# Kernel tuning notes

Hardware: AMD Instinct MI355X
Metric: run time of the kernel (lower is better)

Reference implementation:

```python
import jax, jax.numpy as jnp
import numpy as np

B, T, I, H, O = 128, 512, 128, 2048, 10

def setup_inputs() -> dict:
    key = jax.random.key(0)
    k = jax.random.split(key, 6)
    # xavier-uniform-like scales
    def xav(key, shape):
        fan_in, fan_out = shape[0], shape[1]
        lim = np.sqrt(6.0 / (fan_in + fan_out)).astype(np.float32)
        return jax.random.uniform(key, shape, jnp.float32, -lim, lim)
    return {
        "x": jax.random.normal(k[0], (B, T, I), jnp.float32),
        "W_hx": xav(k[1], (I, H)),
        "W_hh": xav(k[2], (H, H)),
        "b_h": jnp.zeros((H,), jnp.float32),
        "W_ph": xav(k[3], (H, O)),
        "b_o": jnp.zeros((O,), jnp.float32),
    }

def reference(x, W_hx, W_hh, b_h, W_ph, b_o):
    # x: [B, T, I] -> scan over time, recurrent tanh cell
    xt_seq = jnp.swapaxes(x, 0, 1)  # [T, B, I]
    h0 = jnp.zeros((x.shape[0], W_hh.shape[0]), x.dtype)

    def step(h, xt):
        h_new = jnp.tanh(xt @ W_hx + h @ W_hh + b_h)
        return h_new, None

    h_T, _ = jax.lax.scan(step, h0, xt_seq)
    logits = h_T @ W_ph + b_o  # [B, O]
    return jax.nn.softmax(logits, axis=-1)
```

## Files before the change

kernel.cpp:

```cpp
#include <hip/hip_runtime.h>
#include <stdint.h>


#define B_   128
#define T_   512
#define I_   128
#define H_   2048
#define O_   10
#define KK   2176
#define NWG  256
#define NTHR 512

typedef __attribute__((ext_vector_type(8))) _Float16 f16x8;
typedef __attribute__((ext_vector_type(4))) float    f32x4;
typedef __attribute__((ext_vector_type(4))) int      i32x4;

__device__ __forceinline__ float f16_to_f(unsigned short u) {
    return (float)__builtin_bit_cast(_Float16, u);
}
__device__ __forceinline__ unsigned short f_to_f16(float f) {
    return __builtin_bit_cast(unsigned short, (_Float16)f);
}

__device__ __forceinline__ void st64cc(unsigned short* p, uint64_t v) {
    asm volatile("global_store_dwordx2 %0, %1, off sc0 sc1"
                 :: "v"((uint64_t)(uintptr_t)p), "v"(v) : "memory");
}
__device__ __forceinline__ void stflag(unsigned int* p, uint32_t v) {
    asm volatile("global_store_dword %0, %1, off sc0 sc1"
                 :: "v"((uint64_t)(uintptr_t)p), "v"(v) : "memory");
}
__device__ __forceinline__ uint32_t ldflag(const unsigned int* p) {
    uint32_t v;
    asm volatile("global_load_dword %0, %1, off sc0 sc1"
                 : "=v"(v) : "v"((uint64_t)(uintptr_t)p) : "memory");
    asm volatile("s_waitcnt vmcnt(0)" ::: "memory");
    __builtin_amdgcn_sched_barrier(0);
    return v;
}

#define MFMA16(a, b, c) __builtin_amdgcn_mfma_f32_16x16x32_f16((a), (b), (c), 0, 0, 0)

__global__ void prep_init(unsigned int* flags) {
    for (int i = threadIdx.x; i < 8192; i += blockDim.x) flags[i] = 0u;
}

__global__ void prep_weights(const float* __restrict__ Whh, const float* __restrict__ Whx,
                             unsigned short* __restrict__ Wt) {
    __shared__ float tile[32][33];
    const int kt = blockIdx.x;
    const int nt = blockIdx.y;
    const int tx = threadIdx.x & 31;
    const int ty = threadIdx.x >> 5;
#pragma unroll
    for (int r = ty; r < 32; r += 8) {
        const int k = kt * 32 + r;
        const int n = nt * 32 + tx;
        tile[r][tx] = (k < H_) ? Whh[(size_t)k * H_ + n] : Whx[(size_t)(k - H_) * H_ + n];
    }
    __syncthreads();
#pragma unroll
    for (int r = ty; r < 32; r += 8) {
        const int n = nt * 32 + r;
        const int k = kt * 32 + tx;
        Wt[(size_t)n * KK + k] = f_to_f16(tile[tx][r]);
    }
}

__global__ __launch_bounds__(NTHR, 2) void rnn_scan(
    const float* __restrict__ x,
    const unsigned short* __restrict__ Wt,
    const float* __restrict__ b_h,
    const float* __restrict__ W_ph,
    const float* __restrict__ b_o,
    unsigned short* __restrict__ h0,
    unsigned short* __restrict__ h1,
    float* __restrict__ out,
    unsigned int* __restrict__ flags)
{
    const int tid  = threadIdx.x;
    const int wg   = blockIdx.x;
    const int w    = tid >> 6;
    const int lane = tid & 63;
    const int l15  = lane & 15;
    const int l4   = lane >> 4;
    const int rb   = wg >> 5;
    const int cb   = wg & 31;
    const int r0   = rb * 16;
    const int c0   = cb * 64;
    const int arow = r0 + l15;

    unsigned int* gslots = flags + 16 + (size_t)(rb * 32) * 16;
    unsigned int* myslot = gslots + (size_t)cb * 16;
    unsigned int* prodslot = gslots + (size_t)((w * 4 + (lane & 3)) * 16);

    __shared__ f32x4 red[8][4][64];
    __shared__ unsigned short hT[16][68];
    __shared__ float epi[128];
    __shared__ float lgt[16];

    i32x4 wh[4][8];
    i32x4 wx[4];
#pragma unroll
    for (int n = 0; n < 4; ++n) {
        const size_t colbase = (size_t)(c0 + n * 16 + l15) * KK;
#pragma unroll
        for (int j = 0; j < 8; ++j)
            wh[n][j] = *(const i32x4*)(Wt + colbase + (size_t)(w * 256 + j * 32 + l4 * 8));
        if (w >= 4)
            wx[n] = *(const i32x4*)(Wt + colbase + (size_t)(2048 + (w - 4) * 32 + l4 * 8));
    }

    const int rn   = tid >> 6;
    const int rL   = tid & 63;
    const int lcol = rn * 16 + (rL & 15);
    const int lr0  = (rL >> 4) * 4;
    const float rbias = b_h[c0 + lcol];
    const int slr = tid >> 4;
    const int scg = tid & 15;

    for (int t = 0; t < T_; ++t) {
        const unsigned short* rh  = (t & 1) ? h0 : h1;
        unsigned short*       whp = (t & 1) ? h1 : h0;

        f32x4 acc[4];
#pragma unroll
        for (int n = 0; n < 4; ++n) acc[n] = f32x4{0.f, 0.f, 0.f, 0.f};

        if (w >= 4) {
            const float* xp = x + ((size_t)arow * T_ + t) * I_ + (size_t)((w - 4) * 32 + l4 * 8);
            const f32x4 xa = *(const f32x4*)xp;
            const f32x4 xb = *(const f32x4*)(xp + 4);
            f16x8 xv;
#pragma unroll
            for (int jj = 0; jj < 8; ++jj)
                xv[jj] = (_Float16)((jj < 4) ? xa[jj] : xb[jj - 4]);
#pragma unroll
            for (int n = 0; n < 4; ++n)
                acc[n] = MFMA16(xv, __builtin_bit_cast(f16x8, wx[n]), acc[n]);
        }

        if (t > 0) {
            for (;;) {
                uint32_t v = 0xFFFFFFFFu;
                if ((lane & ~3) == 0) v = ldflag(prodslot);
                if (__all((int)(v >= (unsigned)t))) break;
            }

            const uint64_t base64 = (uint64_t)(uintptr_t)(rh + (size_t)arow * H_ + (size_t)(w * 256 + l4 * 8));
            i32x4 hb[8];
#define ISSJ(jj, IMM) \
    asm volatile("global_load_dwordx4 %0, %1, off offset:" IMM " sc1" \
                 : "=v"(hb[jj]) : "v"(base64) : "memory")
#define WAITV(NSTR) do { \
    asm volatile("s_waitcnt vmcnt(" NSTR ")" ::: "memory"); \
    __builtin_amdgcn_sched_barrier(0); } while (0)
#define CONS(jj) do { \
    const f16x8 AH = __builtin_bit_cast(f16x8, hb[jj]); \
    acc[0] = MFMA16(AH, __builtin_bit_cast(f16x8, wh[0][jj]), acc[0]); \
    acc[1] = MFMA16(AH, __builtin_bit_cast(f16x8, wh[1][jj]), acc[1]); \
    acc[2] = MFMA16(AH, __builtin_bit_cast(f16x8, wh[2][jj]), acc[2]); \
    acc[3] = MFMA16(AH, __builtin_bit_cast(f16x8, wh[3][jj]), acc[3]); \
    } while (0)
            ISSJ(0, "0");   ISSJ(1, "64");  ISSJ(2, "128"); ISSJ(3, "192");
            ISSJ(4, "256"); ISSJ(5, "320"); ISSJ(6, "384"); ISSJ(7, "448");
            WAITV("7"); CONS(0);
            WAITV("6"); CONS(1);
            WAITV("5"); CONS(2);
            WAITV("4"); CONS(3);
            WAITV("3"); CONS(4);
            WAITV("2"); CONS(5);
            WAITV("1"); CONS(6);
            WAITV("0"); CONS(7);
#undef ISSJ
#undef WAITV
#undef CONS
        }

#pragma unroll
        for (int n = 0; n < 4; ++n) red[w][n][lane] = acc[n];
        __syncthreads();

        if (tid < 256) {
            f32x4 v = red[0][rn][rL];
#pragma unroll
            for (int p = 1; p < 8; ++p) v += red[p][rn][rL];
#pragma unroll
            for (int r = 0; r < 4; ++r)
                hT[lr0 + r][lcol] = f_to_f16(tanhf(v[r] + rbias));
        }
        __syncthreads();

        if (tid < 256) {
            const uint64_t val = *(const uint64_t*)&hT[slr][scg * 4];
            st64cc(whp + (size_t)(r0 + slr) * H_ + (size_t)(c0 + scg * 4), val);
        }
        asm volatile("s_waitcnt vmcnt(0)" ::: "memory");
        __syncthreads();

        if (tid == 0) stflag(myslot, (unsigned)(t + 1));
    }

    if (w == 0) {
        for (;;) {
            uint32_t v = 0xFFFFFFFFu;
            if (lane < 32) v = ldflag(gslots + (size_t)lane * 16);
            if (__all((int)(v >= (unsigned)T_))) break;
        }
    }
    __syncthreads();

    if (cb < 16) {
        const int b = r0 + cb;
        float o[O_];
#pragma unroll
        for (int j = 0; j < O_; ++j) o[j] = 0.f;
        const uint64_t hbase = (uint64_t)(uintptr_t)(h1 + (size_t)b * H_ + (size_t)tid * 4);
        uint64_t hh;
        asm volatile("global_load_dwordx2 %0, %1, off sc1"
                     : "=v"(hh) : "v"(hbase) : "memory");
        asm volatile("s_waitcnt vmcnt(0)" ::: "memory");
        __builtin_amdgcn_sched_barrier(0);
#pragma unroll
        for (int e = 0; e < 4; ++e) {
            const float hv = f16_to_f((unsigned short)(hh >> (16 * e)));
            const float* wrow = W_ph + (size_t)(tid * 4 + e) * O_;
#pragma unroll
            for (int j = 0; j < O_; ++j) o[j] += hv * wrow[j];
        }
#pragma unroll
        for (int off = 32; off > 0; off >>= 1) {
#pragma unroll
            for (int j = 0; j < O_; ++j) o[j] += __shfl_down(o[j], off);
        }
        if (lane == 0) {
#pragma unroll
            for (int j = 0; j < O_; ++j) epi[w * 16 + j] = o[j];
        }
        __syncthreads();
        if (tid < O_) {
            float l = b_o[tid];
#pragma unroll
            for (int ww = 0; ww < 8; ++ww) l += epi[ww * 16 + tid];
            lgt[tid] = l;
        }
        __syncthreads();
        if (tid < O_) {
            float m = lgt[0];
#pragma unroll
            for (int j = 1; j < O_; ++j) m = fmaxf(m, lgt[j]);
            float ssum = 0.f;
#pragma unroll
            for (int j = 0; j < O_; ++j) ssum += expf(lgt[j] - m);
            out[(size_t)b * O_ + tid] = expf(lgt[tid] - m) / ssum;
        }
    }
}

extern "C" void kernel_launch(void* const* d_in, const int* in_sizes, int n_in,
                              void* d_out, int out_size, void* d_ws, size_t ws_size,
                              hipStream_t stream) {
    const float* x    = (const float*)d_in[0];
    const float* Whx  = (const float*)d_in[1];
    const float* Whh  = (const float*)d_in[2];
    const float* bh   = (const float*)d_in[3];
    const float* Wph  = (const float*)d_in[4];
    const float* bo   = (const float*)d_in[5];
    float* out = (float*)d_out;

    char* ws = (char*)d_ws;
    unsigned int*   flags = (unsigned int*)ws;
    unsigned short* Wt    = (unsigned short*)(ws + 32768);
    unsigned short* h0    = Wt + (size_t)H_ * KK;
    unsigned short* h1    = h0 + (size_t)B_ * H_;

    hipLaunchKernelGGL(prep_init, dim3(1), dim3(256), 0, stream, flags);
    hipLaunchKernelGGL(prep_weights, dim3(68, 64), dim3(256), 0, stream, Whh, Whx, Wt);

    void* args[] = {
        (void*)&x, (void*)&Wt, (void*)&bh, (void*)&Wph, (void*)&bo,
        (void*)&h0, (void*)&h1, (void*)&out, (void*)&flags
    };
    hipLaunchCooperativeKernel((const void*)rnn_scan, dim3(NWG), dim3(NTHR), args, 0, stream);
}
```

Measured before the change: 2.141 ms.

## Embed parity tag bits in fp16 hidden state to skip flag polling

Moves from double to triple buffering of the hidden state. Each stored fp16 value carries a parity tag in bit 14, so a consumer can speculatively load h, check the tags, and skip polling the producer flags when all data is already fresh. The h loads are also issued before the x-projection MFMAs so they overlap that work. This depends on tanh outputs having |h|<2, which leaves bit 14 clear in fp16, and on visibility ordering of the cache-coherent stores. A failed tag check falls back to flag polling plus a reload.

```diff
diff --git a/kernel.cpp b/kernel.cpp
--- a/kernel.cpp
+++ b/kernel.cpp
@@ -10,6 +10,8 @@
 #define KK   2176
 #define NWG  256
 #define NTHR 512
+#define TAG2 0x40004000u
+#define MSK2 0xBFFFBFFFu
 
 typedef __attribute__((ext_vector_type(8))) _Float16 f16x8;
 typedef __attribute__((ext_vector_type(4))) float    f32x4;
@@ -24,6 +26,10 @@
 
 __device__ __forceinline__ void st64cc(unsigned short* p, uint64_t v) {
     asm volatile("global_store_dwordx2 %0, %1, off sc0 sc1"
+                 :: "v"((uint64_t)(uintptr_t)p), "v"(v) : "memory");
+}
+__device__ __forceinline__ void st32cc(uint32_t* p, uint32_t v) {
+    asm volatile("global_store_dword %0, %1, off sc0 sc1"
                  :: "v"((uint64_t)(uintptr_t)p), "v"(v) : "memory");
 }
 __device__ __forceinline__ void stflag(unsigned int* p, uint32_t v) {
@@ -41,8 +47,13 @@
 
 #define MFMA16(a, b, c) __builtin_amdgcn_mfma_f32_16x16x32_f16((a), (b), (c), 0, 0, 0)
 
-__global__ void prep_init(unsigned int* flags) {
-    for (int i = threadIdx.x; i < 8192; i += blockDim.x) flags[i] = 0u;
+__global__ void prep_init(unsigned int* flags,
+                          unsigned short* h0, unsigned short* h1, unsigned short* h2) {
+    const int i = blockIdx.x * blockDim.x + threadIdx.x;
+    if (i < 8192) flags[i] = 0u;
+    st32cc((uint32_t*)h0 + i, 0u);
+    st32cc((uint32_t*)h1 + i, 0u);
+    st32cc((uint32_t*)h2 + i, TAG2);
 }
 
 __global__ void prep_weights(const float* __restrict__ Whh, const float* __restrict__ Whx,
@@ -75,6 +86,7 @@
     const float* __restrict__ b_o,
     unsigned short* __restrict__ h0,
     unsigned short* __restrict__ h1,
+    unsigned short* __restrict__ h2,
     float* __restrict__ out,
     unsigned int* __restrict__ flags)
 {
@@ -119,63 +131,93 @@
     const int slr = tid >> 4;
     const int scg = tid & 15;
 
+    unsigned short* cur = h0;
+    unsigned short* nxt = h1;
+    unsigned short* old = h2;
+
     for (int t = 0; t < T_; ++t) {
-        const unsigned short* rh  = (t & 1) ? h0 : h1;
-        unsigned short*       whp = (t & 1) ? h1 : h0;
+        const int par = t & 1;
 
         f32x4 acc[4];
 #pragma unroll
         for (int n = 0; n < 4; ++n) acc[n] = f32x4{0.f, 0.f, 0.f, 0.f};
 
-        if (w >= 4) {
-            const float* xp = x + ((size_t)arow * T_ + t) * I_ + (size_t)((w - 4) * 32 + l4 * 8);
-            const f32x4 xa = *(const f32x4*)xp;
-            const f32x4 xb = *(const f32x4*)(xp + 4);
-            f16x8 xv;
-#pragma unroll
-            for (int jj = 0; jj < 8; ++jj)
-                xv[jj] = (_Float16)((jj < 4) ? xa[jj] : xb[jj - 4]);
-#pragma unroll
-            for (int n = 0; n < 4; ++n)
-                acc[n] = MFMA16(xv, __builtin_bit_cast(f16x8, wx[n]), acc[n]);
-        }
-
-        if (t > 0) {
-            for (;;) {
-                uint32_t v = 0xFFFFFFFFu;
-                if ((lane & ~3) == 0) v = ldflag(prodslot);
-                if (__all((int)(v >= (unsigned)t))) break;
-            }
-
-            const uint64_t base64 = (uint64_t)(uintptr_t)(rh + (size_t)arow * H_ + (size_t)(w * 256 + l4 * 8));
-            i32x4 hb[8];
+        i32x4 hb[8];
+        const uint64_t base64 = (uint64_t)(uintptr_t)(cur + (size_t)arow * H_ + (size_t)(w * 256 + l4 * 8));
+
 #define ISSJ(jj, IMM) \
     asm volatile("global_load_dwordx4 %0, %1, off offset:" IMM " sc1" \
                  : "=v"(hb[jj]) : "v"(base64) : "memory")
+#define ISSALL() do { \
+    ISSJ(0, "0");   ISSJ(1, "64");  ISSJ(2, "128"); ISSJ(3, "192"); \
+    ISSJ(4, "256"); ISSJ(5, "320"); ISSJ(6, "384"); ISSJ(7, "448"); } while (0)
 #define WAITV(NSTR) do { \
     asm volatile("s_waitcnt vmcnt(" NSTR ")" ::: "memory"); \
     __builtin_amdgcn_sched_barrier(0); } while (0)
-#define CONS(jj) do { \
+#define STRIPJ(jj) do { if (par) { \
+    hb[jj][0] = (int)((uint32_t)hb[jj][0] & MSK2); \
+    hb[jj][1] = (int)((uint32_t)hb[jj][1] & MSK2); \
+    hb[jj][2] = (int)((uint32_t)hb[jj][2] & MSK2); \
+    hb[jj][3] = (int)((uint32_t)hb[jj][3] & MSK2); } } while (0)
+#define CONSJ(jj) do { \
     const f16x8 AH = __builtin_bit_cast(f16x8, hb[jj]); \
     acc[0] = MFMA16(AH, __builtin_bit_cast(f16x8, wh[0][jj]), acc[0]); \
     acc[1] = MFMA16(AH, __builtin_bit_cast(f16x8, wh[1][jj]), acc[1]); \
     acc[2] = MFMA16(AH, __builtin_bit_cast(f16x8, wh[2][jj]), acc[2]); \
     acc[3] = MFMA16(AH, __builtin_bit_cast(f16x8, wh[3][jj]), acc[3]); \
     } while (0)
-            ISSJ(0, "0");   ISSJ(1, "64");  ISSJ(2, "128"); ISSJ(3, "192");
-            ISSJ(4, "256"); ISSJ(5, "320"); ISSJ(6, "384"); ISSJ(7, "448");
-            WAITV("7"); CONS(0);
-            WAITV("6"); CONS(1);
-            WAITV("5"); CONS(2);
-            WAITV("4"); CONS(3);
-            WAITV("3"); CONS(4);
-            WAITV("2"); CONS(5);
-            WAITV("1"); CONS(6);
-            WAITV("0"); CONS(7);
+
+        if (t > 0) ISSALL();
+
+        if (w >= 4) {
+            const float* xp = x + ((size_t)arow * T_ + t) * I_ + (size_t)((w - 4) * 32 + l4 * 8);
+            const f32x4 xa = *(const f32x4*)xp;
+            const f32x4 xb = *(const f32x4*)(xp + 4);
+            f16x8 xv;
+#pragma unroll
+            for (int jj = 0; jj < 8; ++jj)
+                xv[jj] = (_Float16)((jj < 4) ? xa[jj] : xb[jj - 4]);
+#pragma unroll
+            for (int n = 0; n < 4; ++n)
+                acc[n] = MFMA16(xv, __builtin_bit_cast(f16x8, wx[n]), acc[n]);
+        }
+
+        if (t > 0) {
+            WAITV("0");
+            uint32_t andv = 0xFFFFFFFFu, orv = 0u;
+#pragma unroll
+            for (int j = 0; j < 8; ++j) {
+                const uint32_t d0 = (uint32_t)hb[j][0], d1 = (uint32_t)hb[j][1];
+                const uint32_t d2 = (uint32_t)hb[j][2], d3 = (uint32_t)hb[j][3];
+                andv &= (d0 & d1 & d2 & d3);
+                orv  |= (d0 | d1 | d2 | d3);
+            }
+            const int ok = par ? ((andv & TAG2) == TAG2) : ((orv & TAG2) == 0u);
+            if (__all(ok)) {
+#pragma unroll
+                for (int j = 0; j < 8; ++j) { STRIPJ(j); CONSJ(j); }
+            } else {
+                for (;;) {
+                    uint32_t v = 0xFFFFFFFFu;
+                    if ((lane & ~3) == 0) v = ldflag(prodslot);
+                    if (__all((int)(v >= (unsigned)t))) break;
+                }
+                ISSALL();
+                WAITV("7"); STRIPJ(0); CONSJ(0);
+                WAITV("6"); STRIPJ(1); CONSJ(1);
+                WAITV("5"); STRIPJ(2); CONSJ(2);
+                WAITV("4"); STRIPJ(3); CONSJ(3);
+                WAITV("3"); STRIPJ(4); CONSJ(4);
+                WAITV("2"); STRIPJ(5); CONSJ(5);
+                WAITV("1"); STRIPJ(6); CONSJ(6);
+                WAITV("0"); STRIPJ(7); CONSJ(7);
+            }
+        }
 #undef ISSJ
+#undef ISSALL
 #undef WAITV
-#undef CONS
-        }
+#undef STRIPJ
+#undef CONSJ
 
 #pragma unroll
         for (int n = 0; n < 4; ++n) red[w][n][lane] = acc[n];
@@ -185,20 +227,24 @@
             f32x4 v = red[0][rn][rL];
 #pragma unroll
             for (int p = 1; p < 8; ++p) v += red[p][rn][rL];
+            const unsigned int tagbit = (unsigned int)((t + 1) & 1) << 14;
 #pragma unroll
             for (int r = 0; r < 4; ++r)
-                hT[lr0 + r][lcol] = f_to_f16(tanhf(v[r] + rbias));
+                hT[lr0 + r][lcol] = (unsigned short)(f_to_f16(tanhf(v[r] + rbias)) | tagbit);
         }
         __syncthreads();
 
         if (tid < 256) {
             const uint64_t val = *(const uint64_t*)&hT[slr][scg * 4];
-            st64cc(whp + (size_t)(r0 + slr) * H_ + (size_t)(c0 + scg * 4), val);
+            st64cc(nxt + (size_t)(r0 + slr) * H_ + (size_t)(c0 + scg * 4), val);
         }
         asm volatile("s_waitcnt vmcnt(0)" ::: "memory");
         __syncthreads();
 
         if (tid == 0) stflag(myslot, (unsigned)(t + 1));
+
+        unsigned short* tmp = cur;
+        cur = nxt; nxt = old; old = tmp;
     }
 
     if (w == 0) {
@@ -212,15 +258,15 @@
 
     if (cb < 16) {
         const int b = r0 + cb;
-        float o[O_];
-#pragma unroll
-        for (int j = 0; j < O_; ++j) o[j] = 0.f;
-        const uint64_t hbase = (uint64_t)(uintptr_t)(h1 + (size_t)b * H_ + (size_t)tid * 4);
+        const uint64_t hbase = (uint64_t)(uintptr_t)(h2 + (size_t)b * H_ + (size_t)tid * 4);
         uint64_t hh;
         asm volatile("global_load_dwordx2 %0, %1, off sc1"
                      : "=v"(hh) : "v"(hbase) : "memory");
         asm volatile("s_waitcnt vmcnt(0)" ::: "memory");
         __builtin_amdgcn_sched_barrier(0);
+        float o[O_];
+#pragma unroll
+        for (int j = 0; j < O_; ++j) o[j] = 0.f;
 #pragma unroll
         for (int e = 0; e < 4; ++e) {
             const float hv = f16_to_f((unsigned short)(hh >> (16 * e)));
@@ -273,13 +319,14 @@
     unsigned short* Wt    = (unsigned short*)(ws + 32768);
     unsigned short* h0    = Wt + (size_t)H_ * KK;
     unsigned short* h1    = h0 + (size_t)B_ * H_;
-
-    hipLaunchKernelGGL(prep_init, dim3(1), dim3(256), 0, stream, flags);
+    unsigned short* h2    = h1 + (size_t)B_ * H_;
+
+    hipLaunchKernelGGL(prep_init, dim3(512), dim3(256), 0, stream, flags, h0, h1, h2);
     hipLaunchKernelGGL(prep_weights, dim3(68, 64), dim3(256), 0, stream, Whh, Whx, Wt);
 
     void* args[] = {
         (void*)&x, (void*)&Wt, (void*)&bh, (void*)&Wph, (void*)&bo,
-        (void*)&h0, (void*)&h1, (void*)&out, (void*)&flags
+        (void*)&h0, (void*)&h1, (void*)&h2, (void*)&out, (void*)&flags
     };
     hipLaunchCooperativeKernel((const void*)rnn_scan, dim3(NWG), dim3(NTHR), args, 0, stream);
 }
```

Result: slower. 2.956 ms (+38.1%).
